# Performance work log

Measured on AMD Instinct MI355X. Metric: run time of the kernel, lower is better.

The kernel has to match this reference:

```python
import jax, jax.numpy as jnp
import numpy as np

C = 256  # in_dims
CQ = C // 2


def setup_inputs() -> dict:
    key = jax.random.key(0)
    ks = jax.random.split(key, 8)
    B, H, W = 8, 64, 64
    x = jax.random.normal(ks[0], (B, C, H, W), dtype=jnp.float32)
    s = 0.02
    Wq = jax.random.normal(ks[1], (CQ, C), dtype=jnp.float32) * s
    bq = jax.random.normal(ks[2], (CQ,), dtype=jnp.float32) * s
    Wk = jax.random.normal(ks[3], (CQ, C), dtype=jnp.float32) * s
    bk = jax.random.normal(ks[4], (CQ,), dtype=jnp.float32) * s
    Wv = jax.random.normal(ks[5], (C, C), dtype=jnp.float32) * s
    bv = jax.random.normal(ks[6], (C,), dtype=jnp.float32) * s
    gamma = jax.random.normal(ks[7], (1,), dtype=jnp.float32) * 0.5  # torch inits to 0; use nonzero for a meaningful test
    return {"x": x, "Wq": Wq, "bq": bq, "Wk": Wk, "bk": bk, "Wv": Wv, "bv": bv, "gamma": gamma}


def reference(x, Wq, bq, Wk, bk, Wv, bv, gamma):
    B, Ch, H, W = x.shape
    N = H * W
    xf = x.reshape(B, Ch, N)  # 1x1 conv == per-pixel linear over channels
    q = jnp.einsum('oc,bcn->bon', Wq, xf) + bq[None, :, None]  # [B, C/2, N]
    k = jnp.einsum('oc,bcn->bon', Wk, xf) + bk[None, :, None]  # [B, C/2, N]
    v = jnp.einsum('oc,bcn->bon', Wv, xf) + bv[None, :, None]  # [B, C,   N]
    # attention[b, m, n] = q_m . k_n ; softmax over dim=1 (the m axis), matching nn.Softmax(dim=1)
    scores = jnp.einsum('bcm,bcn->bmn', q, k)  # [B, N, N]
    attn = jax.nn.softmax(scores, axis=1)
    # torch.bmm(V, A^T)[b,c,m] = sum_n V[b,c,n] * A[b,m,n]
    out = jnp.einsum('bcn,bmn->bcm', v, attn)  # [B, C, N]
    return gamma * out.reshape(B, Ch, H, W) + x
```

## Files before the change

kernel.cpp:

```cpp
#include <hip/hip_runtime.h>


typedef unsigned short u16;
typedef __attribute__((ext_vector_type(8))) short bf16x8;
typedef __attribute__((ext_vector_type(4))) short bf16x4;
typedef __attribute__((ext_vector_type(4))) float f32x4;

__device__ __forceinline__ float bf2f(u16 u) {
  union { unsigned int i; float f; } v; v.i = ((unsigned int)u) << 16; return v.f;
}
__device__ __forceinline__ u16 f2bf(float f) {
  union { float f; unsigned int i; } v; v.f = f;
  unsigned int r = v.i + 0x7fffu + ((v.i >> 16) & 1u);
  return (u16)(r >> 16);
}

#define NB 8
#define NC 256
#define NCQ 128
#define NN 4096
#define LOG2E 1.4426950408889634f

__device__ __forceinline__ int scan_bad(const u16* p, int ns, int tid) {
  int bad = 0;
  for (int i = tid; i < ns; i += 256) {
    const int e = (p[2 * i] >> 7) & 0xff;
    bad |= (e >= 0x90) ? 1 : 0;
  }
  return bad;
}

__device__ __forceinline__ bf16x8 load8(const u16* pb, const float* pf,
                                        size_t off, bool f) {
  if (!f) return *(const bf16x8*)(pb + off);
  const float4 a = *(const float4*)(pf + off);
  const float4 b = *(const float4*)(pf + off + 4);
  bf16x8 r;
  r[0] = (short)f2bf(a.x); r[1] = (short)f2bf(a.y);
  r[2] = (short)f2bf(a.z); r[3] = (short)f2bf(a.w);
  r[4] = (short)f2bf(b.x); r[5] = (short)f2bf(b.y);
  r[6] = (short)f2bf(b.z); r[7] = (short)f2bf(b.w);
  return r;
}

__global__ __launch_bounds__(256, 2) void qkv_kernel(
    const void* xv, const void* Wqv, const void* bqv, const void* Wkv,
    const void* bkv, const void* Wvv, const void* bvv,
    u16* __restrict__ q2T, u16* __restrict__ kT, u16* __restrict__ vout) {
  __shared__ __align__(16) u16 xT[64][264];
  __shared__ int fl[8];
  const int tid = threadIdx.x;
  const int bid = blockIdx.x;
  const int b = bid & 7, n0 = (bid >> 3) << 6;

  if (tid < 8) fl[tid] = 0;
  __syncthreads();
  if (scan_bad((const u16*)xv, 256, tid)) fl[0] = 1;
  if (scan_bad((const u16*)Wqv, 64, tid)) fl[1] = 1;
  if (scan_bad((const u16*)Wkv, 64, tid)) fl[2] = 1;
  if (scan_bad((const u16*)Wvv, 64, tid)) fl[3] = 1;
  if (scan_bad((const u16*)bqv, 64, tid)) fl[4] = 1;
  if (scan_bad((const u16*)bkv, 64, tid)) fl[5] = 1;
  if (scan_bad((const u16*)bvv, 64, tid)) fl[6] = 1;
  __syncthreads();
  const bool fx = fl[0] != 0;

  {
    const int c = tid;
    const size_t roff = (size_t)(b * NC + c) * NN + n0;
    if (fx) {
      const float* xp = (const float*)xv + roff;
#pragma unroll
      for (int j = 0; j < 16; ++j) {
        const float4 t = *(const float4*)(xp + j * 4);
        xT[j * 4 + 0][c] = f2bf(t.x); xT[j * 4 + 1][c] = f2bf(t.y);
        xT[j * 4 + 2][c] = f2bf(t.z); xT[j * 4 + 3][c] = f2bf(t.w);
      }
    } else {
      const u16* xp = (const u16*)xv + roff;
#pragma unroll
      for (int j = 0; j < 8; ++j) {
        bf16x8 t = *(const bf16x8*)(xp + j * 8);
#pragma unroll
        for (int e = 0; e < 8; ++e) xT[j * 8 + e][c] = (u16)t[e];
      }
    }
  }
  __syncthreads();

  const int w = tid >> 6, lane = tid & 63, l15 = lane & 15, quad = lane >> 4;
  const u16* Wb; const float* Wf; const u16* Bb; const float* Bf;
  bool fW, fB; int obase = 0; u16* dstT = nullptr; float sc = 1.f;
  if (w == 0) {
    Wb = (const u16*)Wqv; Wf = (const float*)Wqv;
    Bb = (const u16*)bqv; Bf = (const float*)bqv;
    fW = fl[1]; fB = fl[4]; dstT = q2T; sc = LOG2E;
  } else if (w == 1) {
    Wb = (const u16*)Wkv; Wf = (const float*)Wkv;
    Bb = (const u16*)bkv; Bf = (const float*)bkv;
    fW = fl[2]; fB = fl[5]; dstT = kT;
  } else if (w == 2) {
    Wb = (const u16*)Wvv; Wf = (const float*)Wvv;
    Bb = (const u16*)bvv; Bf = (const float*)bvv;
    fW = fl[3]; fB = fl[6];
  } else {
    Wb = (const u16*)Wvv + 32768; Wf = (const float*)Wvv + 32768;
    Bb = (const u16*)bvv + 128;   Bf = (const float*)bvv + 128;
    fW = fl[3]; fB = fl[6]; obase = 128;
  }

  bf16x8 xfr[4][8];
#pragma unroll
  for (int nt = 0; nt < 4; ++nt) {
    const u16* xp = &xT[nt * 16 + l15][quad * 8];
#pragma unroll
    for (int ks = 0; ks < 8; ++ks) xfr[nt][ks] = *(const bf16x8*)(xp + ks * 32);
  }

  for (int ot = 0; ot < 8; ++ot) {
    bf16x8 wfr[8];
    const size_t wrow = (size_t)(ot * 16 + l15) * 256 + quad * 8;
#pragma unroll
    for (int ks = 0; ks < 8; ++ks) wfr[ks] = load8(Wb, Wf, wrow + ks * 32, fW);
    float bias[4];
    {
      const int boff = ot * 16 + quad * 4;
#pragma unroll
      for (int r = 0; r < 4; ++r)
        bias[r] = fB ? Bf[boff + r] : bf2f(Bb[boff + r]);
    }
#pragma unroll
    for (int nt = 0; nt < 4; ++nt) {
      f32x4 acc = {0.f, 0.f, 0.f, 0.f};
#pragma unroll
      for (int ks = 0; ks < 8; ++ks)
        acc = __builtin_amdgcn_mfma_f32_16x16x32_bf16(wfr[ks], xfr[nt][ks], acc, 0, 0, 0);
      const int n = n0 + nt * 16 + l15;
      if (w < 2) {
        ushort4 st;
        st.x = f2bf((acc[0] + bias[0]) * sc); st.y = f2bf((acc[1] + bias[1]) * sc);
        st.z = f2bf((acc[2] + bias[2]) * sc); st.w = f2bf((acc[3] + bias[3]) * sc);
        *(ushort4*)(dstT + ((size_t)(b * NN + n)) * NCQ + ot * 16 + quad * 4) = st;
      } else {
        const int c = obase + ot * 16 + quad * 4;
#pragma unroll
        for (int r = 0; r < 4; ++r)
          vout[((size_t)(b * NC + c + r)) * NN + n] = f2bf(acc[r] + bias[r]);
      }
    }
  }
}

__global__ __launch_bounds__(256, 2) void stats_kernel(
    const u16* __restrict__ q2T, const u16* __restrict__ kT,
    float* __restrict__ rbuf) {
  __shared__ float zbuf[4][64];
  const int bid = blockIdx.x;
  const int b = bid & 7, n0 = (bid >> 3) << 6;
  const int tid = threadIdx.x;
  const int w = tid >> 6, lane = tid & 63, l15 = lane & 15, quad = lane >> 4;

  bf16x8 kf[4][4];
  {
    const u16* kp = kT + ((size_t)(b * NN + n0 + l15)) * NCQ + quad * 8;
#pragma unroll
    for (int nt = 0; nt < 4; ++nt)
#pragma unroll
      for (int ks = 0; ks < 4; ++ks) {
        kf[nt][ks] = *(const bf16x8*)(kp + (size_t)(nt * 16) * NCQ + ks * 32);
        asm volatile("" : "+v"(kf[nt][ks]));
      }
  }

  const u16* qbase = q2T + ((size_t)(b * NN + w * 1024 + l15)) * NCQ + quad * 8;
  float Z[4] = {0.f, 0.f, 0.f, 0.f};
  bf16x8 afA[4], afB[4];
#pragma unroll
  for (int ks = 0; ks < 4; ++ks) afA[ks] = *(const bf16x8*)(qbase + ks * 32);

  for (int it = 0; it < 64; it += 2) {
    {
      const u16* qp = qbase + (size_t)((it + 1) * 16) * NCQ;
#pragma unroll
      for (int ks = 0; ks < 4; ++ks) afB[ks] = *(const bf16x8*)(qp + ks * 32);
    }
#pragma unroll
    for (int nt = 0; nt < 4; ++nt) {
      f32x4 acc = {0.f, 0.f, 0.f, 0.f};
#pragma unroll
      for (int ks = 0; ks < 4; ++ks)
        acc = __builtin_amdgcn_mfma_f32_16x16x32_bf16(afA[ks], kf[nt][ks], acc, 0, 0, 0);
      Z[nt] += __builtin_amdgcn_exp2f(acc[0]) + __builtin_amdgcn_exp2f(acc[1]) +
               __builtin_amdgcn_exp2f(acc[2]) + __builtin_amdgcn_exp2f(acc[3]);
    }
    {
      const int it2 = (it + 2) & 63;
      const u16* qp = qbase + (size_t)(it2 * 16) * NCQ;
#pragma unroll
      for (int ks = 0; ks < 4; ++ks) afA[ks] = *(const bf16x8*)(qp + ks * 32);
    }
#pragma unroll
    for (int nt = 0; nt < 4; ++nt) {
      f32x4 acc = {0.f, 0.f, 0.f, 0.f};
#pragma unroll
      for (int ks = 0; ks < 4; ++ks)
        acc = __builtin_amdgcn_mfma_f32_16x16x32_bf16(afB[ks], kf[nt][ks], acc, 0, 0, 0);
      Z[nt] += __builtin_amdgcn_exp2f(acc[0]) + __builtin_amdgcn_exp2f(acc[1]) +
               __builtin_amdgcn_exp2f(acc[2]) + __builtin_amdgcn_exp2f(acc[3]);
    }
  }
#pragma unroll
  for (int nt = 0; nt < 4; ++nt) {
    float z = Z[nt];
    z += __shfl_xor(z, 16, 64);
    z += __shfl_xor(z, 32, 64);
    Z[nt] = z;
  }
  if (lane < 16) {
#pragma unroll
    for (int nt = 0; nt < 4; ++nt) zbuf[w][nt * 16 + lane] = Z[nt];
  }
  __syncthreads();
  if (tid < 64) {
    const float z = zbuf[0][tid] + zbuf[1][tid] + zbuf[2][tid] + zbuf[3][tid];
    rbuf[b * NN + n0 + tid] = 1.0f / z;
  }
}

__global__ __launch_bounds__(256, 4) void scale_kernel(
    u16* __restrict__ vr, const float* __restrict__ rbuf) {
  const int flat = (blockIdx.x * 256 + threadIdx.x) * 8;
  const int n = flat & (NN - 1);
  const int b = flat >> 20;
  const float4 r0 = *(const float4*)(rbuf + (b << 12) + n);
  const float4 r1 = *(const float4*)(rbuf + (b << 12) + n + 4);
  const ushort4 a0 = *(const ushort4*)(vr + flat);
  const ushort4 a1 = *(const ushort4*)(vr + flat + 4);
  ushort4 s0, s1;
  s0.x = f2bf(bf2f(a0.x) * r0.x); s0.y = f2bf(bf2f(a0.y) * r0.y);
  s0.z = f2bf(bf2f(a0.z) * r0.z); s0.w = f2bf(bf2f(a0.w) * r0.w);
  s1.x = f2bf(bf2f(a1.x) * r1.x); s1.y = f2bf(bf2f(a1.y) * r1.y);
  s1.z = f2bf(bf2f(a1.z) * r1.z); s1.w = f2bf(bf2f(a1.w) * r1.w);
  *(ushort4*)(vr + flat) = s0;
  *(ushort4*)(vr + flat + 4) = s1;
}

__global__ __launch_bounds__(256, 4) void out_kernel(
    const u16* __restrict__ q2T, const u16* __restrict__ kT,
    const u16* __restrict__ vr,
    const void* xv, const void* gv,
    const void* bqv, const void* bkv, const void* bvv,
    void* outv) {
  __shared__ __align__(16) u16 qs[64][136];
  __shared__ __align__(16) u16 et[2][4][16][68];
  __shared__ int fl[2];
  const int tid = threadIdx.x;
  if (tid < 2) fl[tid] = 0;
  __syncthreads();
  if (scan_bad((const u16*)xv, 256, tid)) fl[0] = 1;
  if (scan_bad((const u16*)bqv, 64, tid) | scan_bad((const u16*)bkv, 64, tid) |
      scan_bad((const u16*)bvv, 64, tid)) fl[1] = 1;

  const int bid = blockIdx.x;
  const int b = bid & 7;
  const int r7 = bid >> 3;
  const int ch = r7 & 1;
  const int m0 = (r7 >> 1) << 6;
  const int w = tid >> 6, lane = tid & 63, l15 = lane & 15, quad = lane >> 4;

  {
    const int mm = tid >> 2, ck = (tid & 3) * 32;
    const u16* src = q2T + ((size_t)(b * NN + m0 + mm)) * NCQ + ck;
#pragma unroll
    for (int j = 0; j < 4; ++j)
      *(bf16x8*)(&qs[mm][ck + j * 8]) = *(const bf16x8*)(src + j * 8);
  }
  __syncthreads();
  const bool fx = fl[0] != 0, fg = fl[1] != 0;

  f32x4 acc[8];
#pragma unroll
  for (int i = 0; i < 8; ++i) acc[i] = (f32x4){0.f, 0.f, 0.f, 0.f};

  const u16* kb = kT + ((size_t)(b * NN + w * 16 + l15)) * NCQ + quad * 8;
  const u16* vb = vr + ((size_t)(b * NC + ch * 128 + w * 32 + l15)) * NN + quad * 8;

  bf16x8 kfA[4], kfB[4];
#pragma unroll
  for (int ks = 0; ks < 4; ++ks)
    kfA[ks] = *(const bf16x8*)(kb + ks * 32);

  for (int n0 = 0; n0 < NN; n0 += 128) {
    {
      bf16x8 vf[4];
#pragma unroll
      for (int ct = 0; ct < 2; ++ct)
#pragma unroll
        for (int ns = 0; ns < 2; ++ns)
          vf[ct * 2 + ns] =
              *(const bf16x8*)(vb + (size_t)(ct * 16) * NN + n0 + ns * 32);
#pragma unroll
      for (int ks = 0; ks < 4; ++ks)
        kfB[ks] = *(const bf16x8*)(kb + (size_t)(n0 + 64) * NCQ + ks * 32);
#pragma unroll
      for (int mg = 0; mg < 4; ++mg) {
        f32x4 s = {0.f, 0.f, 0.f, 0.f};
#pragma unroll
        for (int ks = 0; ks < 4; ++ks) {
          const bf16x8 qfr =
              *(const bf16x8*)(&qs[mg * 16 + l15][quad * 8 + ks * 32]);
          s = __builtin_amdgcn_mfma_f32_16x16x32_bf16(kfA[ks], qfr, s, 0, 0, 0);
        }
        bf16x4 ev;
        ev[0] = (short)f2bf(__builtin_amdgcn_exp2f(s[0]));
        ev[1] = (short)f2bf(__builtin_amdgcn_exp2f(s[1]));
        ev[2] = (short)f2bf(__builtin_amdgcn_exp2f(s[2]));
        ev[3] = (short)f2bf(__builtin_amdgcn_exp2f(s[3]));
        *(bf16x4*)(&et[0][mg][l15][w * 16 + quad * 4]) = ev;
      }
      __syncthreads();
#pragma unroll
      for (int mg = 0; mg < 4; ++mg)
#pragma unroll
        for (int ns = 0; ns < 2; ++ns) {
          const bf16x8 af = *(const bf16x8*)(&et[0][mg][l15][ns * 32 + quad * 8]);
#pragma unroll
          for (int ct = 0; ct < 2; ++ct)
            acc[mg * 2 + ct] = __builtin_amdgcn_mfma_f32_16x16x32_bf16(
                af, vf[ct * 2 + ns], acc[mg * 2 + ct], 0, 0, 0);
        }
    }
    {
      const int n1 = n0 + 64;
      bf16x8 vf[4];
#pragma unroll
      for (int ct = 0; ct < 2; ++ct)
#pragma unroll
        for (int ns = 0; ns < 2; ++ns)
          vf[ct * 2 + ns] =
              *(const bf16x8*)(vb + (size_t)(ct * 16) * NN + n1 + ns * 32);
      {
        const int n2 = (n0 + 128) & (NN - 1);
#pragma unroll
        for (int ks = 0; ks < 4; ++ks)
          kfA[ks] = *(const bf16x8*)(kb + (size_t)n2 * NCQ + ks * 32);
      }
#pragma unroll
      for (int mg = 0; mg < 4; ++mg) {
        f32x4 s = {0.f, 0.f, 0.f, 0.f};
#pragma unroll
        for (int ks = 0; ks < 4; ++ks) {
          const bf16x8 qfr =
              *(const bf16x8*)(&qs[mg * 16 + l15][quad * 8 + ks * 32]);
          s = __builtin_amdgcn_mfma_f32_16x16x32_bf16(kfB[ks], qfr, s, 0, 0, 0);
        }
        bf16x4 ev;
        ev[0] = (short)f2bf(__builtin_amdgcn_exp2f(s[0]));
        ev[1] = (short)f2bf(__builtin_amdgcn_exp2f(s[1]));
        ev[2] = (short)f2bf(__builtin_amdgcn_exp2f(s[2]));
        ev[3] = (short)f2bf(__builtin_amdgcn_exp2f(s[3]));
        *(bf16x4*)(&et[1][mg][l15][w * 16 + quad * 4]) = ev;
      }
      __syncthreads();
#pragma unroll
      for (int mg = 0; mg < 4; ++mg)
#pragma unroll
        for (int ns = 0; ns < 2; ++ns) {
          const bf16x8 af = *(const bf16x8*)(&et[1][mg][l15][ns * 32 + quad * 8]);
#pragma unroll
          for (int ct = 0; ct < 2; ++ct)
            acc[mg * 2 + ct] = __builtin_amdgcn_mfma_f32_16x16x32_bf16(
                af, vf[ct * 2 + ns], acc[mg * 2 + ct], 0, 0, 0);
        }
    }
  }

  const float g = fg ? ((const float*)gv)[0] : bf2f(((const u16*)gv)[0]);
#pragma unroll
  for (int mg = 0; mg < 4; ++mg)
#pragma unroll
    for (int ct = 0; ct < 2; ++ct) {
      const int c = ch * 128 + w * 32 + ct * 16 + l15;
      const int m = m0 + mg * 16 + quad * 4;
      const size_t base = ((size_t)(b * NC + c)) * NN + m;
      const f32x4 a = acc[mg * 2 + ct];
      if (fx) {
        const float4 xl = *(const float4*)((const float*)xv + base);
        float4 st;
        st.x = g * a[0] + xl.x; st.y = g * a[1] + xl.y;
        st.z = g * a[2] + xl.z; st.w = g * a[3] + xl.w;
        *(float4*)((float*)outv + base) = st;
      } else {
        const ushort4 xl = *(const ushort4*)((const u16*)xv + base);
        ushort4 st;
        st.x = f2bf(g * a[0] + bf2f(xl.x));
        st.y = f2bf(g * a[1] + bf2f(xl.y));
        st.z = f2bf(g * a[2] + bf2f(xl.z));
        st.w = f2bf(g * a[3] + bf2f(xl.w));
        *(ushort4*)((u16*)outv + base) = st;
      }
    }
}

extern "C" void kernel_launch(void* const* d_in, const int* in_sizes, int n_in,
                              void* d_out, int out_size, void* d_ws, size_t ws_size,
                              hipStream_t stream) {
  const size_t NEED = 33554432u;
  if (ws_size < NEED) return;

  char* ws = (char*)d_ws;
  u16* q2 = (u16*)(ws);
  u16* kk = (u16*)(ws + 8388608);
  u16* vv = (u16*)(ws + 16777216);
  float* rbuf = (ws_size >= NEED + 131072u) ? (float*)(ws + NEED) : (float*)d_out;

  qkv_kernel<<<512, 256, 0, stream>>>(d_in[0], d_in[1], d_in[2], d_in[3],
                                      d_in[4], d_in[5], d_in[6], q2, kk, vv);
  stats_kernel<<<512, 256, 0, stream>>>(q2, kk, rbuf);
  scale_kernel<<<4096, 256, 0, stream>>>(vv, rbuf);
  out_kernel<<<1024, 256, 0, stream>>>(q2, kk, vv, d_in[0], d_in[7],
                                       d_in[2], d_in[4], d_in[6], d_out);
}
```

Before: 438.4 us.

## Software-pipeline S and PV phases across tiles with one barrier per step

```diff
diff --git a/kernel.cpp b/kernel.cpp
--- a/kernel.cpp
+++ b/kernel.cpp
@@ -20,6 +20,12 @@
 #define NCQ 128
 #define NN 4096
 #define LOG2E 1.4426950408889634f
+
+__device__ __forceinline__ void seg_barrier() {
+  asm volatile("s_waitcnt lgkmcnt(0)" ::: "memory");
+  __builtin_amdgcn_sched_barrier(0);
+  __builtin_amdgcn_s_barrier();
+}
 
 __device__ __forceinline__ int scan_bad(const u16* p, int ns, int tid) {
   int bad = 0;
@@ -285,95 +291,79 @@
   const u16* kb = kT + ((size_t)(b * NN + w * 16 + l15)) * NCQ + quad * 8;
   const u16* vb = vr + ((size_t)(b * NC + ch * 128 + w * 32 + l15)) * NN + quad * 8;
 
-  bf16x8 kfA[4], kfB[4];
+  auto S_phase = [&](int pp, const bf16x8* kf) {
+#pragma unroll
+    for (int mg = 0; mg < 4; ++mg) {
+      f32x4 s = {0.f, 0.f, 0.f, 0.f};
+#pragma unroll
+      for (int ks = 0; ks < 4; ++ks) {
+        const bf16x8 qfr =
+            *(const bf16x8*)(&qs[mg * 16 + l15][quad * 8 + ks * 32]);
+        s = __builtin_amdgcn_mfma_f32_16x16x32_bf16(kf[ks], qfr, s, 0, 0, 0);
+      }
+      bf16x4 ev;
+      ev[0] = (short)f2bf(__builtin_amdgcn_exp2f(s[0]));
+      ev[1] = (short)f2bf(__builtin_amdgcn_exp2f(s[1]));
+      ev[2] = (short)f2bf(__builtin_amdgcn_exp2f(s[2]));
+      ev[3] = (short)f2bf(__builtin_amdgcn_exp2f(s[3]));
+      *(bf16x4*)(&et[pp][mg][l15][w * 16 + quad * 4]) = ev;
+    }
+  };
+  auto PV_phase = [&](int pr, const bf16x8* vf) {
+#pragma unroll
+    for (int mg = 0; mg < 4; ++mg)
+#pragma unroll
+      for (int ns = 0; ns < 2; ++ns) {
+        const bf16x8 af =
+            *(const bf16x8*)(&et[pr][mg][l15][ns * 32 + quad * 8]);
+#pragma unroll
+        for (int ct = 0; ct < 2; ++ct)
+          acc[mg * 2 + ct] = __builtin_amdgcn_mfma_f32_16x16x32_bf16(
+              af, vf[ct * 2 + ns], acc[mg * 2 + ct], 0, 0, 0);
+      }
+  };
+
+  bf16x8 kc[4], kn[4], vf[4];
+#pragma unroll
+  for (int ks = 0; ks < 4; ++ks) kc[ks] = *(const bf16x8*)(kb + ks * 32);
+  S_phase(0, kc);
 #pragma unroll
   for (int ks = 0; ks < 4; ++ks)
-    kfA[ks] = *(const bf16x8*)(kb + ks * 32);
-
-  for (int n0 = 0; n0 < NN; n0 += 128) {
+    kn[ks] = *(const bf16x8*)(kb + (size_t)64 * NCQ + ks * 32);
+  seg_barrier();
+#pragma unroll
+  for (int ks = 0; ks < 4; ++ks) kc[ks] = kn[ks];
+
+#pragma unroll 2
+  for (int t = 1; t < 64; ++t) {
+    const int pp = t & 1;
+    const int nv = (t - 1) * 64;
+#pragma unroll
+    for (int ct = 0; ct < 2; ++ct)
+#pragma unroll
+      for (int ns = 0; ns < 2; ++ns)
+        vf[ct * 2 + ns] =
+            *(const bf16x8*)(vb + (size_t)(ct * 16) * NN + nv + ns * 32);
     {
-      bf16x8 vf[4];
-#pragma unroll
-      for (int ct = 0; ct < 2; ++ct)
-#pragma unroll
-        for (int ns = 0; ns < 2; ++ns)
-          vf[ct * 2 + ns] =
-              *(const bf16x8*)(vb + (size_t)(ct * 16) * NN + n0 + ns * 32);
+      const int tn = (t < 63) ? (t + 1) : 0;
 #pragma unroll
       for (int ks = 0; ks < 4; ++ks)
-        kfB[ks] = *(const bf16x8*)(kb + (size_t)(n0 + 64) * NCQ + ks * 32);
-#pragma unroll
-      for (int mg = 0; mg < 4; ++mg) {
-        f32x4 s = {0.f, 0.f, 0.f, 0.f};
-#pragma unroll
-        for (int ks = 0; ks < 4; ++ks) {
-          const bf16x8 qfr =
-              *(const bf16x8*)(&qs[mg * 16 + l15][quad * 8 + ks * 32]);
-          s = __builtin_amdgcn_mfma_f32_16x16x32_bf16(kfA[ks], qfr, s, 0, 0, 0);
-        }
-        bf16x4 ev;
-        ev[0] = (short)f2bf(__builtin_amdgcn_exp2f(s[0]));
-        ev[1] = (short)f2bf(__builtin_amdgcn_exp2f(s[1]));
-        ev[2] = (short)f2bf(__builtin_amdgcn_exp2f(s[2]));
-        ev[3] = (short)f2bf(__builtin_amdgcn_exp2f(s[3]));
-        *(bf16x4*)(&et[0][mg][l15][w * 16 + quad * 4]) = ev;
-      }
-      __syncthreads();
-#pragma unroll
-      for (int mg = 0; mg < 4; ++mg)
-#pragma unroll
-        for (int ns = 0; ns < 2; ++ns) {
-          const bf16x8 af = *(const bf16x8*)(&et[0][mg][l15][ns * 32 + quad * 8]);
-#pragma unroll
-          for (int ct = 0; ct < 2; ++ct)
-            acc[mg * 2 + ct] = __builtin_amdgcn_mfma_f32_16x16x32_bf16(
-                af, vf[ct * 2 + ns], acc[mg * 2 + ct], 0, 0, 0);
-        }
-    }
-    {
-      const int n1 = n0 + 64;
-      bf16x8 vf[4];
-#pragma unroll
-      for (int ct = 0; ct < 2; ++ct)
-#pragma unroll
-        for (int ns = 0; ns < 2; ++ns)
-          vf[ct * 2 + ns] =
-              *(const bf16x8*)(vb + (size_t)(ct * 16) * NN + n1 + ns * 32);
-      {
-        const int n2 = (n0 + 128) & (NN - 1);
-#pragma unroll
-        for (int ks = 0; ks < 4; ++ks)
-          kfA[ks] = *(const bf16x8*)(kb + (size_t)n2 * NCQ + ks * 32);
-      }
-#pragma unroll
-      for (int mg = 0; mg < 4; ++mg) {
-        f32x4 s = {0.f, 0.f, 0.f, 0.f};
-#pragma unroll
-        for (int ks = 0; ks < 4; ++ks) {
-          const bf16x8 qfr =
-              *(const bf16x8*)(&qs[mg * 16 + l15][quad * 8 + ks * 32]);
-          s = __builtin_amdgcn_mfma_f32_16x16x32_bf16(kfB[ks], qfr, s, 0, 0, 0);
-        }
-        bf16x4 ev;
-        ev[0] = (short)f2bf(__builtin_amdgcn_exp2f(s[0]));
-        ev[1] = (short)f2bf(__builtin_amdgcn_exp2f(s[1]));
-        ev[2] = (short)f2bf(__builtin_amdgcn_exp2f(s[2]));
-        ev[3] = (short)f2bf(__builtin_amdgcn_exp2f(s[3]));
-        *(bf16x4*)(&et[1][mg][l15][w * 16 + quad * 4]) = ev;
-      }
-      __syncthreads();
-#pragma unroll
-      for (int mg = 0; mg < 4; ++mg)
-#pragma unroll
-        for (int ns = 0; ns < 2; ++ns) {
-          const bf16x8 af = *(const bf16x8*)(&et[1][mg][l15][ns * 32 + quad * 8]);
-#pragma unroll
-          for (int ct = 0; ct < 2; ++ct)
-            acc[mg * 2 + ct] = __builtin_amdgcn_mfma_f32_16x16x32_bf16(
-                af, vf[ct * 2 + ns], acc[mg * 2 + ct], 0, 0, 0);
-        }
-    }
-  }
+        kn[ks] = *(const bf16x8*)(kb + (size_t)(tn * 64) * NCQ + ks * 32);
+    }
+    S_phase(pp, kc);
+    PV_phase(pp ^ 1, vf);
+    seg_barrier();
+#pragma unroll
+    for (int ks = 0; ks < 4; ++ks) kc[ks] = kn[ks];
+  }
+
+#pragma unroll
+  for (int ct = 0; ct < 2; ++ct)
+#pragma unroll
+    for (int ns = 0; ns < 2; ++ns)
+      vf[ct * 2 + ns] =
+          *(const bf16x8*)(vb + (size_t)(ct * 16) * NN + 63 * 64 + ns * 32);
+  PV_phase(1, vf);
 
   const float g = fg ? ((const float*)gv)[0] : bf2f(((const u16*)gv)[0]);
 #pragma unroll
```

Measured after the change: 434.3 us. About the same (-0.9%).
